# Performance work log

Measured on AMD Instinct MI355X. Metric: run time of the kernel, lower is better.

## Reference

```python
import jax, jax.numpy as jnp
import numpy as np

B, C, H, W = 16, 512, 64, 64
NH = 8  # num_heads


def setup_inputs() -> dict:
    key = jax.random.key(0)
    ks = jax.random.split(key, 7)
    s = 1.0 / np.sqrt(C)
    return {
        "x": jax.random.normal(ks[0], (B, C, H, W), dtype=jnp.float32),
        "wq": jax.random.normal(ks[1], (C, C), dtype=jnp.float32) * s,
        "bq": jax.random.normal(ks[2], (C,), dtype=jnp.float32) * 0.01,
        "wk": jax.random.normal(ks[3], (C, C), dtype=jnp.float32) * s,
        "bk": jax.random.normal(ks[4], (C,), dtype=jnp.float32) * 0.01,
        "wv": jax.random.normal(ks[5], (C, C), dtype=jnp.float32) * s,
        "bv": jax.random.normal(ks[6], (C,), dtype=jnp.float32) * 0.01,
    }


def reference(x, wq, bq, wk, bk, wv, bv):
    b, c_in, h, w = x.shape
    hd = c_in // NH  # head dim

    def conv1x1(wt, bias):
        # 1x1 conv == channel GEMM: (b,c,h,w) x (o,c) -> (b,o,h,w)
        y = jnp.einsum("bchw,oc->bohw", x, wt) + bias[None, :, None, None]
        # view(b, nh, hd, h, w).permute(0,1,3,4,2) -> (b, nh, h, w, hd)
        return y.reshape(b, NH, hd, h, w).transpose(0, 1, 3, 4, 2)

    q = conv1x1(wq, bq)
    k = conv1x1(wk, bk)
    v = conv1x1(wv, bv)

    # attention along the width axis, per (batch, head, row)
    energy = jnp.einsum("bnhqc,bnhkc->bnhqk", q, k)  # (b,nh,h,w,w)
    attn = jax.nn.softmax(energy, axis=-1)
    out = jnp.einsum("bnhqk,bnhkc->bnhqc", attn, v)  # (b,nh,h,w,hd)

    # permute(0,1,4,2,3) -> (b,nh,hd,h,w) -> view(b, C, h, w)
    out = out.transpose(0, 1, 4, 2, 3).reshape(b, c_in, h, w)
    return out + x
```

## Files before the change

### kernel.cpp

```cpp
#include <hip/hip_runtime.h>
#include <stdint.h>

#define B_   16
#define C_   512
#define H_   64
#define W_   64
#define NH_  8
#define HD_  64
#define HW_  4096

typedef __attribute__((ext_vector_type(8))) _Float16 f16x8;
typedef __attribute__((ext_vector_type(8))) unsigned short u16x8;
typedef __attribute__((ext_vector_type(4))) unsigned short u16x4;
typedef __attribute__((ext_vector_type(4))) float f32x4;

static __device__ __forceinline__ unsigned short f2h(float f) {
  _Float16 h = (_Float16)f;
  unsigned short u;
  __builtin_memcpy(&u, &h, 2);
  return u;
}

static __device__ __forceinline__ void gld_lds16(const void* g, void* l) {
  __builtin_amdgcn_global_load_lds((__attribute__((address_space(1))) void*)g,
                                   (__attribute__((address_space(3))) void*)l,
                                   16, 0, 0);
}

__global__ __launch_bounds__(256) void rcca_tr(const float* __restrict__ x,
                                               unsigned short* __restrict__ xT) {
  __shared__ float lT[64 * 65];
  const int bid = blockIdx.x;
  const int st = bid & 63;
  const int ct = (bid >> 6) & 7;
  const int b  = bid >> 9;
  const int t = threadIdx.x;
  const int hwl = t & 63;
  const int cl0 = (t >> 6) * 16;
  const float* src = x + ((size_t)(b * C_ + ct * 64 + cl0)) * HW_ + st * 64 + hwl;
#pragma unroll
  for (int jj = 0; jj < 16; ++jj)
    lT[(cl0 + jj) * 65 + hwl] = src[(size_t)jj * HW_];
  __syncthreads();
  const int hw2 = t >> 2;
  const int cc0 = (t & 3) * 16;
  u16x8 o0, o1;
#pragma unroll
  for (int u = 0; u < 8; ++u) {
    o0[u] = f2h(lT[(cc0 + u) * 65 + hw2]);
    o1[u] = f2h(lT[(cc0 + 8 + u) * 65 + hw2]);
  }
  unsigned short* dst = xT + ((size_t)b * HW_ + st * 64 + hw2) * C_ + ct * 64 + cc0;
  *(u16x8*)dst = o0;
  *(u16x8*)(dst + 8) = o1;
}

__global__ __launch_bounds__(256) void rcca_cvtw(const float* __restrict__ wq,
                                                 const float* __restrict__ wk,
                                                 const float* __restrict__ wv,
                                                 unsigned short* __restrict__ Wc) {
  const int i = blockIdx.x * 256 + threadIdx.x;
  const int e = i * 4;
  const float* w = (e < 262144) ? wq : (e < 524288) ? wk : wv;
  const int off = e & 262143;
  const float4 v = *(const float4*)(w + off);
  u16x4 p;
  p[0] = f2h(v.x); p[1] = f2h(v.y); p[2] = f2h(v.z); p[3] = f2h(v.w);
  *(u16x4*)(Wc + e) = p;
}

__global__ __launch_bounds__(256) void rcca_gemm(const unsigned short* __restrict__ xT,
                                                 const unsigned short* __restrict__ Wc,
                                                 const float* __restrict__ bq,
                                                 const float* __restrict__ bk,
                                                 const float* __restrict__ bv,
                                                 unsigned short* __restrict__ qkv) {
  __shared__ __align__(16) char gsm[34816];
  unsigned short* lA = (unsigned short*)gsm;
  unsigned short* lB = (unsigned short*)(gsm + 16384);
  unsigned short* sT = (unsigned short*)gsm;
  const int bid = blockIdx.x;
  const int nt = bid % 12;
  const int mt = (bid / 12) & 31;
  const int b  = bid / (12 * 32);
  const int t = threadIdx.x;
  const int wid = t >> 6, lane = t & 63, r = lane & 15, q = lane >> 4;
  const int rx = r & 7;
  const int wm = wid >> 1, wn = wid & 1;
  const unsigned short* Abase = xT + ((size_t)b * HW_ + mt * 128) * C_;
  const unsigned short* Bbase = Wc + (size_t)nt * 128 * C_;
  const int arow = t >> 3;
  const int acol = (((t & 7) ^ ((t >> 3) & 7)) * 8);
  char* lAb = (char*)lA;
  char* lBb = (char*)lB;
  const int wbase = wid * 1024;
  f32x4 acc[4][4];
#pragma unroll
  for (int i = 0; i < 4; ++i)
#pragma unroll
    for (int j = 0; j < 4; ++j)
      acc[i][j] = (f32x4){0.f, 0.f, 0.f, 0.f};

  for (int k0 = 0; k0 < C_; k0 += 64) {
    __syncthreads();
#pragma unroll
    for (int rr = 0; rr < 4; ++rr) {
      gld_lds16(Abase + (size_t)(rr * 32 + arow) * C_ + k0 + acol, lAb + rr * 4096 + wbase);
      gld_lds16(Bbase + (size_t)(rr * 32 + arow) * C_ + k0 + acol, lBb + rr * 4096 + wbase);
    }
    __syncthreads();
#pragma unroll
    for (int kk = 0; kk < 64; kk += 32) {
      const int cbase = kk >> 3;
      f16x8 av[4], bw[4];
#pragma unroll
      for (int i = 0; i < 4; ++i)
        av[i] = *(const f16x8*)&lA[(wm * 64 + i * 16 + r) * 64 + (((cbase + q) ^ rx) * 8)];
#pragma unroll
      for (int j = 0; j < 4; ++j)
        bw[j] = *(const f16x8*)&lB[(wn * 64 + j * 16 + r) * 64 + (((cbase + q) ^ rx) * 8)];
#pragma unroll
      for (int i = 0; i < 4; ++i)
#pragma unroll
        for (int j = 0; j < 4; ++j)
          acc[i][j] = __builtin_amdgcn_mfma_f32_16x16x32_f16(av[i], bw[j], acc[i][j], 0, 0, 0);
    }
  }
  __syncthreads();
  const int headq = nt * 2 + wn;
  const int qsel = headq >> 3;
  const int head = headq & 7;
  const float* bias = (qsel == 0) ? bq : (qsel == 1) ? bk : bv;
#pragma unroll
  for (int j = 0; j < 4; ++j) {
    const float bias_v = bias[head * 64 + j * 16 + r];
#pragma unroll
    for (int i = 0; i < 4; ++i) {
#pragma unroll
      for (int reg = 0; reg < 4; ++reg) {
        const int m = wm * 64 + i * 16 + q * 4 + reg;
        const int n = wn * 64 + j * 16 + r;
        sT[m * 136 + n] = f2h(acc[i][j][reg] + bias_v);
      }
    }
  }
  __syncthreads();
  const int wr = t >> 1, half = t & 1;
  const int hq2 = nt * 2 + half;
  const int qs2 = hq2 >> 3;
  const int hd2 = hq2 & 7;
  const int h2 = mt * 2 + (wr >> 6);
  const int w2 = wr & 63;
  unsigned short* dstb = qkv + (size_t)qs2 * ((size_t)B_ * NH_ * H_ * W_ * HD_)
                       + (((size_t)b * NH_ + hd2) * H_ + h2) * (size_t)(W_ * HD_)
                       + (size_t)w2 * HD_;
#pragma unroll
  for (int u = 0; u < 8; ++u)
    *(u16x8*)(dstb + u * 8) = *(const u16x8*)&sT[wr * 136 + half * 64 + u * 8];
}

__global__ __launch_bounds__(256) void rcca_attn(const unsigned short* __restrict__ Qb,
                                                 const unsigned short* __restrict__ Kb,
                                                 const unsigned short* __restrict__ Vb,
                                                 const float* __restrict__ x,
                                                 float* __restrict__ out) {
  __shared__ __align__(16) char smem[36864];
  unsigned short* sQ = (unsigned short*)smem;
  unsigned short* sK = (unsigned short*)(smem + 9216);
  unsigned short* sV = (unsigned short*)(smem + 18432);
  unsigned short* sP = (unsigned short*)(smem + 27648);
  float* sO = (float*)smem;
  const int bid = blockIdx.x;
  const int h = bid & 63, head = (bid >> 6) & 7, b = bid >> 9;
  const size_t base = (((size_t)b * NH_ + head) * H_ + h) * (size_t)(W_ * HD_);
  const int t = threadIdx.x;
  {
    const int w = t >> 2, c0 = (t & 3) * 16;
    const size_t off = base + (size_t)t * 16;
    u16x8 a0 = *(const u16x8*)(Qb + off);
    u16x8 a1 = *(const u16x8*)(Qb + off + 8);
    *(u16x8*)&sQ[w * 72 + c0] = a0;
    *(u16x8*)&sQ[w * 72 + c0 + 8] = a1;
    u16x8 k0v = *(const u16x8*)(Kb + off);
    u16x8 k1v = *(const u16x8*)(Kb + off + 8);
    *(u16x8*)&sK[w * 72 + c0] = k0v;
    *(u16x8*)&sK[w * 72 + c0 + 8] = k1v;
    const int wv2 = t & 63, cv0 = (t >> 6) * 16;
    const size_t voff = base + (size_t)wv2 * HD_ + cv0;
    u16x8 v0 = *(const u16x8*)(Vb + voff);
    u16x8 v1 = *(const u16x8*)(Vb + voff + 8);
#pragma unroll
    for (int jj = 0; jj < 8; ++jj) {
      sV[(cv0 + jj) * 72 + wv2] = v0[jj];
      sV[(cv0 + 8 + jj) * 72 + wv2] = v1[jj];
    }
  }
  __syncthreads();
  const int wv = t >> 6, lane = t & 63, r = lane & 15, q = lane >> 4;
  f32x4 s[4];
#pragma unroll
  for (int j = 0; j < 4; ++j) s[j] = (f32x4){0.f, 0.f, 0.f, 0.f};
#pragma unroll
  for (int kk = 0; kk < 64; kk += 32) {
    f16x8 aq = *(const f16x8*)&sQ[(wv * 16 + r) * 72 + kk + q * 8];
#pragma unroll
    for (int j = 0; j < 4; ++j) {
      f16x8 bk8 = *(const f16x8*)&sK[(j * 16 + r) * 72 + kk + q * 8];
      s[j] = __builtin_amdgcn_mfma_f32_16x16x32_f16(aq, bk8, s[j], 0, 0, 0);
    }
  }
  float inv[4];
#pragma unroll
  for (int reg = 0; reg < 4; ++reg) {
    float mx = fmaxf(fmaxf(s[0][reg], s[1][reg]), fmaxf(s[2][reg], s[3][reg]));
#pragma unroll
    for (int o = 1; o < 16; o <<= 1) mx = fmaxf(mx, __shfl_xor(mx, o, 64));
    float p0 = __expf(s[0][reg] - mx);
    float p1 = __expf(s[1][reg] - mx);
    float p2 = __expf(s[2][reg] - mx);
    float p3 = __expf(s[3][reg] - mx);
    float sum = p0 + p1 + p2 + p3;
#pragma unroll
    for (int o = 1; o < 16; o <<= 1) sum += __shfl_xor(sum, o, 64);
    inv[reg] = 1.0f / sum;
    const int row = wv * 16 + q * 4 + reg;
    sP[row * 72 + 0 + r]  = f2h(p0);
    sP[row * 72 + 16 + r] = f2h(p1);
    sP[row * 72 + 32 + r] = f2h(p2);
    sP[row * 72 + 48 + r] = f2h(p3);
  }
  __syncthreads();
  f32x4 o4[4];
#pragma unroll
  for (int j = 0; j < 4; ++j) o4[j] = (f32x4){0.f, 0.f, 0.f, 0.f};
#pragma unroll
  for (int kk = 0; kk < 64; kk += 32) {
    f16x8 ap = *(const f16x8*)&sP[(wv * 16 + r) * 72 + kk + q * 8];
#pragma unroll
    for (int jd = 0; jd < 4; ++jd) {
      f16x8 bv8 = *(const f16x8*)&sV[(jd * 16 + r) * 72 + kk + q * 8];
      o4[jd] = __builtin_amdgcn_mfma_f32_16x16x32_f16(ap, bv8, o4[jd], 0, 0, 0);
    }
  }
#pragma unroll
  for (int jd = 0; jd < 4; ++jd) {
    const int d = jd * 16 + r;
#pragma unroll
    for (int reg = 0; reg < 4; ++reg) {
      const int w = wv * 16 + q * 4 + reg;
      sO[d * 66 + w] = o4[jd][reg] * inv[reg];
    }
  }
  __syncthreads();
  const int d = t >> 2, w0 = (t & 3) * 16;
  const size_t obase = ((size_t)b * C_ + head * 64 + d) * HW_ + h * 64 + w0;
  const float4* xr = (const float4*)(x + obase);
  float4* op = (float4*)(out + obase);
#pragma unroll
  for (int u = 0; u < 4; ++u) {
    float4 xv = xr[u];
    float4 ov;
    ov.x = sO[d * 66 + w0 + u * 4 + 0] + xv.x;
    ov.y = sO[d * 66 + w0 + u * 4 + 1] + xv.y;
    ov.z = sO[d * 66 + w0 + u * 4 + 2] + xv.z;
    ov.w = sO[d * 66 + w0 + u * 4 + 3] + xv.w;
    op[u] = ov;
  }
}

extern "C" void kernel_launch(void* const* d_in, const int* in_sizes, int n_in,
                              void* d_out, int out_size, void* d_ws, size_t ws_size,
                              hipStream_t stream) {
  const float* x  = (const float*)d_in[0];
  const float* wq = (const float*)d_in[1];
  const float* bq = (const float*)d_in[2];
  const float* wk = (const float*)d_in[3];
  const float* bk = (const float*)d_in[4];
  const float* wv = (const float*)d_in[5];
  const float* bv = (const float*)d_in[6];
  float* out = (float*)d_out;
  char* ws = (char*)d_ws;
  unsigned short* xT = (unsigned short*)ws;
  unsigned short* Wc = (unsigned short*)(ws + (size_t)67108864);
  unsigned short* Qb = (unsigned short*)(ws + (size_t)68681728);
  unsigned short* Kb = Qb + (size_t)33554432;
  unsigned short* Vb = Kb + (size_t)33554432;
  hipLaunchKernelGGL(rcca_tr,   dim3(8192), dim3(256), 0, stream, x, xT);
  hipLaunchKernelGGL(rcca_cvtw, dim3(768),  dim3(256), 0, stream, wq, wk, wv, Wc);
  hipLaunchKernelGGL(rcca_gemm, dim3(6144), dim3(256), 0, stream, xT, Wc, bq, bk, bv, Qb);
  hipLaunchKernelGGL(rcca_attn, dim3(8192), dim3(256), 0, stream, Qb, Kb, Vb, x, out);
}
```

Baseline: 486.5 us.

## Fuse QKV projection GEMM with width-axis attention per head and row pair

Replaces the separate QKV GEMM and attention kernels with one kernel. Each block computes Q, K and V for one head over two image rows (128 pixels by 192 output channels) and keeps them in shared memory, then runs softmax attention and the residual add directly. This removes writing and re-reading the three large fp16 Q/K/V buffers in global memory. In exchange it uses 72 KB of LDS and a 4x6 accumulator tile, which lowers occupancy. The block index is swizzled so that blocks sharing the same x tile are spread across the grid.

```diff
diff --git a/kernel.cpp b/kernel.cpp
--- a/kernel.cpp
+++ b/kernel.cpp
@@ -69,202 +69,181 @@
   *(u16x4*)(Wc + e) = p;
 }
 
-__global__ __launch_bounds__(256) void rcca_gemm(const unsigned short* __restrict__ xT,
-                                                 const unsigned short* __restrict__ Wc,
-                                                 const float* __restrict__ bq,
-                                                 const float* __restrict__ bk,
-                                                 const float* __restrict__ bv,
-                                                 unsigned short* __restrict__ qkv) {
-  __shared__ __align__(16) char gsm[34816];
-  unsigned short* lA = (unsigned short*)gsm;
-  unsigned short* lB = (unsigned short*)(gsm + 16384);
-  unsigned short* sT = (unsigned short*)gsm;
-  const int bid = blockIdx.x;
-  const int nt = bid % 12;
-  const int mt = (bid / 12) & 31;
-  const int b  = bid / (12 * 32);
+__global__ __launch_bounds__(256) void rcca_fused(
+    const unsigned short* __restrict__ xT, const unsigned short* __restrict__ Wc,
+    const float* __restrict__ bq, const float* __restrict__ bk, const float* __restrict__ bv,
+    const float* __restrict__ x, float* __restrict__ out) {
+  __shared__ __align__(16) char smem[73728];
+  unsigned short* lA = (unsigned short*)smem;
+  unsigned short* lB = (unsigned short*)(smem + 16384);
+  const int sbid = blockIdx.x;
+  const int lg = ((sbid & 7) << 9) | (sbid >> 3);
+  const int head = lg & 7;
+  const int bh = lg >> 3;
+  const int b = bh >> 5;
+  const int ht = bh & 31;
   const int t = threadIdx.x;
   const int wid = t >> 6, lane = t & 63, r = lane & 15, q = lane >> 4;
   const int rx = r & 7;
   const int wm = wid >> 1, wn = wid & 1;
-  const unsigned short* Abase = xT + ((size_t)b * HW_ + mt * 128) * C_;
-  const unsigned short* Bbase = Wc + (size_t)nt * 128 * C_;
   const int arow = t >> 3;
-  const int acol = (((t & 7) ^ ((t >> 3) & 7)) * 8);
+  const int acol = ((t & 7) ^ (arow & 7)) * 8;
   char* lAb = (char*)lA;
   char* lBb = (char*)lB;
   const int wbase = wid * 1024;
-  f32x4 acc[4][4];
+  const unsigned short* Abase = xT + ((size_t)b * HW_ + ht * 128) * C_;
+  const unsigned short* Bbase = Wc + (size_t)head * 64 * C_;
+  f32x4 acc[4][6];
 #pragma unroll
   for (int i = 0; i < 4; ++i)
 #pragma unroll
-    for (int j = 0; j < 4; ++j)
-      acc[i][j] = (f32x4){0.f, 0.f, 0.f, 0.f};
+    for (int j = 0; j < 6; ++j) acc[i][j] = (f32x4){0.f, 0.f, 0.f, 0.f};
 
   for (int k0 = 0; k0 < C_; k0 += 64) {
     __syncthreads();
 #pragma unroll
-    for (int rr = 0; rr < 4; ++rr) {
+    for (int rr = 0; rr < 4; ++rr)
       gld_lds16(Abase + (size_t)(rr * 32 + arow) * C_ + k0 + acol, lAb + rr * 4096 + wbase);
-      gld_lds16(Bbase + (size_t)(rr * 32 + arow) * C_ + k0 + acol, lBb + rr * 4096 + wbase);
+#pragma unroll
+    for (int p = 0; p < 6; ++p) {
+      const size_t grow = (size_t)((p >> 1) * 512 + (p & 1) * 32 + arow) * C_;
+      gld_lds16(Bbase + grow + k0 + acol, lBb + p * 4096 + wbase);
     }
     __syncthreads();
 #pragma unroll
     for (int kk = 0; kk < 64; kk += 32) {
-      const int cbase = kk >> 3;
-      f16x8 av[4], bw[4];
+      const int cb = ((kk >> 3) + q) ^ rx;
+      f16x8 av[4], bw[6];
 #pragma unroll
       for (int i = 0; i < 4; ++i)
-        av[i] = *(const f16x8*)&lA[(wm * 64 + i * 16 + r) * 64 + (((cbase + q) ^ rx) * 8)];
-#pragma unroll
-      for (int j = 0; j < 4; ++j)
-        bw[j] = *(const f16x8*)&lB[(wn * 64 + j * 16 + r) * 64 + (((cbase + q) ^ rx) * 8)];
+        av[i] = *(const f16x8*)&lA[(wm * 64 + i * 16 + r) * 64 + cb * 8];
+#pragma unroll
+      for (int j = 0; j < 6; ++j)
+        bw[j] = *(const f16x8*)&lB[(wn * 96 + j * 16 + r) * 64 + cb * 8];
 #pragma unroll
       for (int i = 0; i < 4; ++i)
 #pragma unroll
-        for (int j = 0; j < 4; ++j)
+        for (int j = 0; j < 6; ++j)
           acc[i][j] = __builtin_amdgcn_mfma_f32_16x16x32_f16(av[i], bw[j], acc[i][j], 0, 0, 0);
     }
   }
   __syncthreads();
-  const int headq = nt * 2 + wn;
-  const int qsel = headq >> 3;
-  const int head = headq & 7;
-  const float* bias = (qsel == 0) ? bq : (qsel == 1) ? bk : bv;
-#pragma unroll
-  for (int j = 0; j < 4; ++j) {
-    const float bias_v = bias[head * 64 + j * 16 + r];
-#pragma unroll
-    for (int i = 0; i < 4; ++i) {
+  unsigned short* sQh = (unsigned short*)(smem + wm * 27648);
+  unsigned short* sKh = (unsigned short*)(smem + wm * 27648 + 9216);
+  unsigned short* sVh = (unsigned short*)(smem + wm * 27648 + 18432);
+#pragma unroll
+  for (int j = 0; j < 6; ++j) {
+    const int n0 = wn * 96 + j * 16;
+    const int sel = n0 >> 6;
+    const int dd = (n0 & 63) + r;
+    const float* bias = (sel == 0) ? bq : (sel == 1) ? bk : bv;
+    const float bias_v = bias[head * 64 + dd];
+    if (sel < 2) {
+      unsigned short* dst = (sel == 0) ? sQh : sKh;
+#pragma unroll
+      for (int i = 0; i < 4; ++i)
+#pragma unroll
+        for (int reg = 0; reg < 4; ++reg)
+          dst[(i * 16 + q * 4 + reg) * 72 + dd] = f2h(acc[i][j][reg] + bias_v);
+    } else {
+#pragma unroll
+      for (int i = 0; i < 4; ++i) {
+        u16x4 pk;
+#pragma unroll
+        for (int reg = 0; reg < 4; ++reg) pk[reg] = f2h(acc[i][j][reg] + bias_v);
+        *(u16x4*)&sVh[dd * 72 + i * 16 + q * 4] = pk;
+      }
+    }
+  }
+  __syncthreads();
+  unsigned short* sPh = (unsigned short*)(smem + 55296 + wm * 9216);
+  f32x4 s2[2][4];
+#pragma unroll
+  for (int i2 = 0; i2 < 2; ++i2)
+#pragma unroll
+    for (int j = 0; j < 4; ++j) s2[i2][j] = (f32x4){0.f, 0.f, 0.f, 0.f};
+#pragma unroll
+  for (int kk = 0; kk < 64; kk += 32) {
+    f16x8 aq0 = *(const f16x8*)&sQh[(wn * 32 + r) * 72 + kk + q * 8];
+    f16x8 aq1 = *(const f16x8*)&sQh[(wn * 32 + 16 + r) * 72 + kk + q * 8];
+#pragma unroll
+    for (int j = 0; j < 4; ++j) {
+      f16x8 bk8 = *(const f16x8*)&sKh[(j * 16 + r) * 72 + kk + q * 8];
+      s2[0][j] = __builtin_amdgcn_mfma_f32_16x16x32_f16(aq0, bk8, s2[0][j], 0, 0, 0);
+      s2[1][j] = __builtin_amdgcn_mfma_f32_16x16x32_f16(aq1, bk8, s2[1][j], 0, 0, 0);
+    }
+  }
+  float inv2[2][4];
+#pragma unroll
+  for (int i2 = 0; i2 < 2; ++i2)
+#pragma unroll
+    for (int reg = 0; reg < 4; ++reg) {
+      float mx = fmaxf(fmaxf(s2[i2][0][reg], s2[i2][1][reg]),
+                       fmaxf(s2[i2][2][reg], s2[i2][3][reg]));
+#pragma unroll
+      for (int o = 1; o < 16; o <<= 1) mx = fmaxf(mx, __shfl_xor(mx, o, 64));
+      float p0 = __expf(s2[i2][0][reg] - mx);
+      float p1 = __expf(s2[i2][1][reg] - mx);
+      float p2 = __expf(s2[i2][2][reg] - mx);
+      float p3 = __expf(s2[i2][3][reg] - mx);
+      float sum = p0 + p1 + p2 + p3;
+#pragma unroll
+      for (int o = 1; o < 16; o <<= 1) sum += __shfl_xor(sum, o, 64);
+      inv2[i2][reg] = 1.0f / sum;
+      const int row = wn * 32 + i2 * 16 + q * 4 + reg;
+      sPh[row * 72 + r] = f2h(p0);
+      sPh[row * 72 + 16 + r] = f2h(p1);
+      sPh[row * 72 + 32 + r] = f2h(p2);
+      sPh[row * 72 + 48 + r] = f2h(p3);
+    }
+  __syncthreads();
+  f32x4 o4[2][4];
+#pragma unroll
+  for (int i2 = 0; i2 < 2; ++i2)
+#pragma unroll
+    for (int jd = 0; jd < 4; ++jd) o4[i2][jd] = (f32x4){0.f, 0.f, 0.f, 0.f};
+#pragma unroll
+  for (int kk = 0; kk < 64; kk += 32) {
+    f16x8 ap0 = *(const f16x8*)&sPh[(wn * 32 + r) * 72 + kk + q * 8];
+    f16x8 ap1 = *(const f16x8*)&sPh[(wn * 32 + 16 + r) * 72 + kk + q * 8];
+#pragma unroll
+    for (int jd = 0; jd < 4; ++jd) {
+      f16x8 bv8 = *(const f16x8*)&sVh[(jd * 16 + r) * 72 + kk + q * 8];
+      o4[0][jd] = __builtin_amdgcn_mfma_f32_16x16x32_f16(ap0, bv8, o4[0][jd], 0, 0, 0);
+      o4[1][jd] = __builtin_amdgcn_mfma_f32_16x16x32_f16(ap1, bv8, o4[1][jd], 0, 0, 0);
+    }
+  }
+  float* sOh = (float*)(smem + wm * 27648);
+#pragma unroll
+  for (int i2 = 0; i2 < 2; ++i2)
+#pragma unroll
+    for (int jd = 0; jd < 4; ++jd) {
+      const int d = jd * 16 + r;
 #pragma unroll
       for (int reg = 0; reg < 4; ++reg) {
-        const int m = wm * 64 + i * 16 + q * 4 + reg;
-        const int n = wn * 64 + j * 16 + r;
-        sT[m * 136 + n] = f2h(acc[i][j][reg] + bias_v);
+        const int w = wn * 32 + i2 * 16 + q * 4 + reg;
+        sOh[d * 66 + w] = o4[i2][jd][reg] * inv2[i2][reg];
       }
     }
-  }
-  __syncthreads();
-  const int wr = t >> 1, half = t & 1;
-  const int hq2 = nt * 2 + half;
-  const int qs2 = hq2 >> 3;
-  const int hd2 = hq2 & 7;
-  const int h2 = mt * 2 + (wr >> 6);
-  const int w2 = wr & 63;
-  unsigned short* dstb = qkv + (size_t)qs2 * ((size_t)B_ * NH_ * H_ * W_ * HD_)
-                       + (((size_t)b * NH_ + hd2) * H_ + h2) * (size_t)(W_ * HD_)
-                       + (size_t)w2 * HD_;
-#pragma unroll
-  for (int u = 0; u < 8; ++u)
-    *(u16x8*)(dstb + u * 8) = *(const u16x8*)&sT[wr * 136 + half * 64 + u * 8];
-}
-
-__global__ __launch_bounds__(256) void rcca_attn(const unsigned short* __restrict__ Qb,
-                                                 const unsigned short* __restrict__ Kb,
-                                                 const unsigned short* __restrict__ Vb,
-                                                 const float* __restrict__ x,
-                                                 float* __restrict__ out) {
-  __shared__ __align__(16) char smem[36864];
-  unsigned short* sQ = (unsigned short*)smem;
-  unsigned short* sK = (unsigned short*)(smem + 9216);
-  unsigned short* sV = (unsigned short*)(smem + 18432);
-  unsigned short* sP = (unsigned short*)(smem + 27648);
-  float* sO = (float*)smem;
-  const int bid = blockIdx.x;
-  const int h = bid & 63, head = (bid >> 6) & 7, b = bid >> 9;
-  const size_t base = (((size_t)b * NH_ + head) * H_ + h) * (size_t)(W_ * HD_);
-  const int t = threadIdx.x;
-  {
-    const int w = t >> 2, c0 = (t & 3) * 16;
-    const size_t off = base + (size_t)t * 16;
-    u16x8 a0 = *(const u16x8*)(Qb + off);
-    u16x8 a1 = *(const u16x8*)(Qb + off + 8);
-    *(u16x8*)&sQ[w * 72 + c0] = a0;
-    *(u16x8*)&sQ[w * 72 + c0 + 8] = a1;
-    u16x8 k0v = *(const u16x8*)(Kb + off);
-    u16x8 k1v = *(const u16x8*)(Kb + off + 8);
-    *(u16x8*)&sK[w * 72 + c0] = k0v;
-    *(u16x8*)&sK[w * 72 + c0 + 8] = k1v;
-    const int wv2 = t & 63, cv0 = (t >> 6) * 16;
-    const size_t voff = base + (size_t)wv2 * HD_ + cv0;
-    u16x8 v0 = *(const u16x8*)(Vb + voff);
-    u16x8 v1 = *(const u16x8*)(Vb + voff + 8);
-#pragma unroll
-    for (int jj = 0; jj < 8; ++jj) {
-      sV[(cv0 + jj) * 72 + wv2] = v0[jj];
-      sV[(cv0 + 8 + jj) * 72 + wv2] = v1[jj];
-    }
-  }
-  __syncthreads();
-  const int wv = t >> 6, lane = t & 63, r = lane & 15, q = lane >> 4;
-  f32x4 s[4];
-#pragma unroll
-  for (int j = 0; j < 4; ++j) s[j] = (f32x4){0.f, 0.f, 0.f, 0.f};
-#pragma unroll
-  for (int kk = 0; kk < 64; kk += 32) {
-    f16x8 aq = *(const f16x8*)&sQ[(wv * 16 + r) * 72 + kk + q * 8];
-#pragma unroll
-    for (int j = 0; j < 4; ++j) {
-      f16x8 bk8 = *(const f16x8*)&sK[(j * 16 + r) * 72 + kk + q * 8];
-      s[j] = __builtin_amdgcn_mfma_f32_16x16x32_f16(aq, bk8, s[j], 0, 0, 0);
-    }
-  }
-  float inv[4];
-#pragma unroll
-  for (int reg = 0; reg < 4; ++reg) {
-    float mx = fmaxf(fmaxf(s[0][reg], s[1][reg]), fmaxf(s[2][reg], s[3][reg]));
-#pragma unroll
-    for (int o = 1; o < 16; o <<= 1) mx = fmaxf(mx, __shfl_xor(mx, o, 64));
-    float p0 = __expf(s[0][reg] - mx);
-    float p1 = __expf(s[1][reg] - mx);
-    float p2 = __expf(s[2][reg] - mx);
-    float p3 = __expf(s[3][reg] - mx);
-    float sum = p0 + p1 + p2 + p3;
-#pragma unroll
-    for (int o = 1; o < 16; o <<= 1) sum += __shfl_xor(sum, o, 64);
-    inv[reg] = 1.0f / sum;
-    const int row = wv * 16 + q * 4 + reg;
-    sP[row * 72 + 0 + r]  = f2h(p0);
-    sP[row * 72 + 16 + r] = f2h(p1);
-    sP[row * 72 + 32 + r] = f2h(p2);
-    sP[row * 72 + 48 + r] = f2h(p3);
-  }
-  __syncthreads();
-  f32x4 o4[4];
-#pragma unroll
-  for (int j = 0; j < 4; ++j) o4[j] = (f32x4){0.f, 0.f, 0.f, 0.f};
-#pragma unroll
-  for (int kk = 0; kk < 64; kk += 32) {
-    f16x8 ap = *(const f16x8*)&sP[(wv * 16 + r) * 72 + kk + q * 8];
-#pragma unroll
-    for (int jd = 0; jd < 4; ++jd) {
-      f16x8 bv8 = *(const f16x8*)&sV[(jd * 16 + r) * 72 + kk + q * 8];
-      o4[jd] = __builtin_amdgcn_mfma_f32_16x16x32_f16(ap, bv8, o4[jd], 0, 0, 0);
-    }
-  }
-#pragma unroll
-  for (int jd = 0; jd < 4; ++jd) {
-    const int d = jd * 16 + r;
-#pragma unroll
-    for (int reg = 0; reg < 4; ++reg) {
-      const int w = wv * 16 + q * 4 + reg;
-      sO[d * 66 + w] = o4[jd][reg] * inv[reg];
-    }
-  }
   __syncthreads();
   const int d = t >> 2, w0 = (t & 3) * 16;
-  const size_t obase = ((size_t)b * C_ + head * 64 + d) * HW_ + h * 64 + w0;
-  const float4* xr = (const float4*)(x + obase);
-  float4* op = (float4*)(out + obase);
-#pragma unroll
-  for (int u = 0; u < 4; ++u) {
-    float4 xv = xr[u];
-    float4 ov;
-    ov.x = sO[d * 66 + w0 + u * 4 + 0] + xv.x;
-    ov.y = sO[d * 66 + w0 + u * 4 + 1] + xv.y;
-    ov.z = sO[d * 66 + w0 + u * 4 + 2] + xv.z;
-    ov.w = sO[d * 66 + w0 + u * 4 + 3] + xv.w;
-    op[u] = ov;
+#pragma unroll
+  for (int hs = 0; hs < 2; ++hs) {
+    const float* sO2 = (const float*)(smem + hs * 27648);
+    const int h = ht * 2 + hs;
+    const size_t obase = (((size_t)b * C_ + head * 64 + d) * H_ + h) * (size_t)W_ + w0;
+    const float4* xr = (const float4*)(x + obase);
+    float4* op = (float4*)(out + obase);
+#pragma unroll
+    for (int u = 0; u < 4; ++u) {
+      float4 xv = xr[u];
+      float4 ov;
+      ov.x = sO2[d * 66 + w0 + u * 4 + 0] + xv.x;
+      ov.y = sO2[d * 66 + w0 + u * 4 + 1] + xv.y;
+      ov.z = sO2[d * 66 + w0 + u * 4 + 2] + xv.z;
+      ov.w = sO2[d * 66 + w0 + u * 4 + 3] + xv.w;
+      op[u] = ov;
+    }
   }
 }
 
@@ -282,11 +261,7 @@
   char* ws = (char*)d_ws;
   unsigned short* xT = (unsigned short*)ws;
   unsigned short* Wc = (unsigned short*)(ws + (size_t)67108864);
-  unsigned short* Qb = (unsigned short*)(ws + (size_t)68681728);
-  unsigned short* Kb = Qb + (size_t)33554432;
-  unsigned short* Vb = Kb + (size_t)33554432;
-  hipLaunchKernelGGL(rcca_tr,   dim3(8192), dim3(256), 0, stream, x, xT);
-  hipLaunchKernelGGL(rcca_cvtw, dim3(768),  dim3(256), 0, stream, wq, wk, wv, Wc);
-  hipLaunchKernelGGL(rcca_gemm, dim3(6144), dim3(256), 0, stream, xT, Wc, bq, bk, bv, Qb);
-  hipLaunchKernelGGL(rcca_attn, dim3(8192), dim3(256), 0, stream, Qb, Kb, Vb, x, out);
-}
+  hipLaunchKernelGGL(rcca_tr,    dim3(8192), dim3(256), 0, stream, x, xT);
+  hipLaunchKernelGGL(rcca_cvtw,  dim3(768),  dim3(256), 0, stream, wq, wk, wv, Wc);
+  hipLaunchKernelGGL(rcca_fused, dim3(4096), dim3(256), 0, stream, xT, Wc, bq, bk, bv, x, out);
+}
```

Measured after the change: 422.9 us. 1.15x faster.
